# Kernel optimization log

Hardware: AMD Instinct MI355X
Metric: run time of the kernel (lower is better)

## Reference

```python
import jax, jax.numpy as jnp
import numpy as np

N_NODES = 100000
N_EDGES = 1600000
DK = 32
OUT_DIM = 32


def setup_inputs() -> dict:
    key = jax.random.key(0)
    ks = jax.random.split(key, 7)
    X = jax.random.normal(ks[0], (N_NODES, DK), dtype=jnp.float32)
    K = jax.random.normal(ks[1], (N_NODES, DK), dtype=jnp.float32)
    V = jax.random.normal(ks[2], (N_NODES, DK), dtype=jnp.float32)
    # output projection (nn.Dense(out_dim)) params
    W_o = jax.random.normal(ks[3], (DK, OUT_DIM), dtype=jnp.float32) / np.sqrt(DK)
    b_o = jnp.zeros((OUT_DIM,), dtype=jnp.float32)
    # sparsity descriptor td: edge list, dst sorted so segment ops see sorted ids
    src = jax.random.randint(ks[4], (N_EDGES,), 0, N_NODES, dtype=jnp.int32)
    dst = jnp.sort(jax.random.randint(ks[5], (N_EDGES,), 0, N_NODES, dtype=jnp.int32))
    return {"X": X, "K": K, "V": V, "W_o": W_o, "b_o": b_o,
            "src": src, "dst": dst, "num_seg": N_NODES}


def reference(X, K, V, W_o, b_o, src, dst, num_seg):
    dk = X.shape[-1]
    # per-edge attention logits: <Q[dst], K[src]> / dk  -> (E,)
    scores = jnp.einsum('ed,ed->e', jnp.take(X, dst, axis=0),
                        jnp.take(K, src, axis=0)) / dk
    # segment (per-neighborhood) softmax over edges sharing a dst node
    seg_max = jax.ops.segment_max(scores, dst, num_segments=num_seg,
                                  indices_are_sorted=True)
    e = jnp.exp(scores - jnp.take(seg_max, dst))
    denom = jax.ops.segment_sum(e, dst, num_segments=num_seg,
                                indices_are_sorted=True)
    alpha = e / jnp.take(denom, dst)  # (E,)
    # weighted aggregation of values, scattered back to nodes -> (N, dk)
    agg = jax.ops.segment_sum(alpha[:, None] * jnp.take(V, src, axis=0), dst,
                              num_segments=num_seg, indices_are_sorted=True)
    # output projection W_o
    return agg @ W_o + b_o
```

## Files before the change

kernel.cpp:

```cpp
#include <hip/hip_runtime.h>
#include <math.h>

#define DK 32
#define OUT_DIM 32

typedef float  f32x4  __attribute__((ext_vector_type(4)));
typedef short  bf16x8 __attribute__((ext_vector_type(8)));

__device__ __forceinline__ unsigned f2bf_rne(float x) {
    unsigned u = __float_as_uint(x);
    return (u + 0x7fffu + ((u >> 16) & 1u)) >> 16;
}

__global__ void prep_kernel(const int* __restrict__ dst,
                            const float* __restrict__ K,
                            const float* __restrict__ V,
                            int E, int N,
                            int* __restrict__ row_ptr,
                            unsigned* __restrict__ KV) {
    const int t = blockIdx.x * blockDim.x + threadIdx.x;
    if (t < E) {
        const int cur  = dst[t];
        const int prev = (t == 0) ? -1 : dst[t - 1];
        for (int j = prev + 1; j <= cur; ++j) row_ptr[j] = t;
        if (t == E - 1) {
            for (int j = cur + 1; j <= N; ++j) row_ptr[j] = E;
        }
    }
    if (t < N * DK) {
        KV[t] = (f2bf_rne(V[t]) << 16) | f2bf_rne(K[t]);
    }
}

__global__ void build_row_ptr_kernel(const int* __restrict__ dst, int E, int N,
                                     int* __restrict__ row_ptr) {
    int e = blockIdx.x * blockDim.x + threadIdx.x;
    if (e >= E) return;
    int cur  = dst[e];
    int prev = (e == 0) ? -1 : dst[e - 1];
    for (int j = prev + 1; j <= cur; ++j) row_ptr[j] = e;
    if (e == E - 1) {
        for (int j = cur + 1; j <= N; ++j) row_ptr[j] = E;
    }
}

__global__ __launch_bounds__(256) void gat_fused_kernel(
    const float* __restrict__ X, const uint4* __restrict__ KV,
    const float* __restrict__ Wo, const float* __restrict__ bo,
    const int* __restrict__ src, const int* __restrict__ row_ptr,
    float* __restrict__ out, int N) {

    __shared__ uint4 s_part[16 * 17];

    const int tid  = threadIdx.x;
    const int w    = tid >> 6;
    const int lane = tid & 63;
    const int g    = lane >> 3;
    const int c    = lane & 7;

    const int n_blk = blockIdx.x * 16;
    const int n_w   = n_blk + w * 4;

    const int rpv = row_ptr[min(n_w + min(lane, 4), N)];

    const float4* X4 = (const float4*)X;
    unsigned* part32 = (unsigned*)s_part;
    const float scale = 0.03125f;

    for (int i = 0; i < 4; ++i) {
        const int begin = __builtin_amdgcn_readlane(rpv, i);
        const int end   = __builtin_amdgcn_readlane(rpv, i + 1);
        const int n     = n_w + i;

        float4 q = X4[min(n, N - 1) * 8 + c];
        q.x *= scale; q.y *= scale; q.z *= scale; q.w *= scale;

        float  l   = 0.0f;
        float4 acc = make_float4(0.f, 0.f, 0.f, 0.f);

        for (int e0 = begin; e0 < end; e0 += 16) {
            const int sa = src[min(e0 + g,     end - 1)];
            const int sb = src[min(e0 + 8 + g, end - 1)];
            const uint4 A = KV[sa * 8 + c];
            const uint4 B = KV[sb * 8 + c];

            float p0 = fmaf(__uint_as_float(A.x << 16), q.x,
                       fmaf(__uint_as_float(A.y << 16), q.y,
                       fmaf(__uint_as_float(A.z << 16), q.z,
                            __uint_as_float(A.w << 16) * q.w)));
            float p1 = fmaf(__uint_as_float(B.x << 16), q.x,
                       fmaf(__uint_as_float(B.y << 16), q.y,
                       fmaf(__uint_as_float(B.z << 16), q.z,
                            __uint_as_float(B.w << 16) * q.w)));
            p0 += __shfl_xor(p0, 1);  p1 += __shfl_xor(p1, 1);
            p0 += __shfl_xor(p0, 2);  p1 += __shfl_xor(p1, 2);
            p0 += __shfl_xor(p0, 4);  p1 += __shfl_xor(p1, 4);

            const float w0 = (e0 + g     < end) ? __expf(p0) : 0.0f;
            const float w1 = (e0 + 8 + g < end) ? __expf(p1) : 0.0f;
            l += w0 + w1;

            acc.x = fmaf(w0, __uint_as_float(A.x & 0xffff0000u), acc.x);
            acc.y = fmaf(w0, __uint_as_float(A.y & 0xffff0000u), acc.y);
            acc.z = fmaf(w0, __uint_as_float(A.z & 0xffff0000u), acc.z);
            acc.w = fmaf(w0, __uint_as_float(A.w & 0xffff0000u), acc.w);
            acc.x = fmaf(w1, __uint_as_float(B.x & 0xffff0000u), acc.x);
            acc.y = fmaf(w1, __uint_as_float(B.y & 0xffff0000u), acc.y);
            acc.z = fmaf(w1, __uint_as_float(B.z & 0xffff0000u), acc.z);
            acc.w = fmaf(w1, __uint_as_float(B.w & 0xffff0000u), acc.w);
        }

        l     += __shfl_xor(l, 8);
        acc.x += __shfl_xor(acc.x, 8);  acc.y += __shfl_xor(acc.y, 8);
        acc.z += __shfl_xor(acc.z, 8);  acc.w += __shfl_xor(acc.w, 8);
        l += __shfl_xor(l, 16);  l += __shfl_xor(l, 32);

        const float inv = (end > begin) ? (1.0f / l) : 0.0f;
        acc.x *= inv; acc.y *= inv; acc.z *= inv; acc.w *= inv;

        if ((g & 1) == 0) {
            const int p   = g >> 1;
            const int row = w * 4 + i;
            const int off = row * 68 + p * 16 + c * 2;
            part32[off]     = f2bf_rne(acc.x) | (f2bf_rne(acc.y) << 16);
            part32[off + 1] = f2bf_rne(acc.z) | (f2bf_rne(acc.w) << 16);
        }
    }

    __syncthreads();

    if (w == 0) {
        const int quad = lane >> 4;
        const int col  = lane & 15;

        union BF { bf16x8 v; unsigned short u[8]; };
        BF bf0, bf1;
#pragma unroll
        for (int j2 = 0; j2 < 8; ++j2) {
            bf0.u[j2] = (unsigned short)f2bf_rne(Wo[(quad * 8 + j2) * OUT_DIM + col]);
            bf1.u[j2] = (unsigned short)f2bf_rne(Wo[(quad * 8 + j2) * OUT_DIM + 16 + col]);
        }
        const float bias0 = bo[col];
        const float bias1 = bo[16 + col];

        union AF { uint4 u; bf16x8 v; };
        f32x4 C0 = {bias0, bias0, bias0, bias0};
        f32x4 C1 = {bias1, bias1, bias1, bias1};
#pragma unroll
        for (int cc = 0; cc < 4; ++cc) {
            AF a;
            a.u = s_part[col * 17 + cc * 4 + quad];
            C0 = __builtin_amdgcn_mfma_f32_16x16x32_bf16(a.v, bf0.v, C0, 0, 0, 0);
            C1 = __builtin_amdgcn_mfma_f32_16x16x32_bf16(a.v, bf1.v, C1, 0, 0, 0);
        }
#pragma unroll
        for (int r = 0; r < 4; ++r) {
            const int n = n_blk + quad * 4 + r;
            if (n < N) {
                out[n * OUT_DIM + col]      = C0[r];
                out[n * OUT_DIM + 16 + col] = C1[r];
            }
        }
    }
}

__global__ __launch_bounds__(256) void gat_node_f32_kernel(
    const float* __restrict__ X, const float* __restrict__ Km,
    const float* __restrict__ Vm, const float* __restrict__ Wo,
    const float* __restrict__ bo, const int* __restrict__ src,
    const int* __restrict__ row_ptr, float* __restrict__ out, int N) {
    const int tid  = threadIdx.x;
    const int wave = tid >> 6;
    const int lane = tid & 63;
    const int g    = lane >> 3;
    const int c    = lane & 7;
    const int j    = lane & 31;
    const int half = lane >> 5;
    const int n = blockIdx.x * 4 + wave;
    if (n >= N) return;
    const int begin = row_ptr[n];
    const int end   = row_ptr[n + 1];
    const float4* X4 = (const float4*)X;
    const float4* K4 = (const float4*)Km;
    const float4* V4 = (const float4*)Vm;
    const float4 q4 = X4[n * 8 + c];
    float  l   = 0.0f;
    float4 acc = make_float4(0.0f, 0.0f, 0.0f, 0.0f);
    for (int e0 = begin; e0 < end; e0 += 16) {
        const int  ea = e0 + g;
        const int  eb = ea + 8;
        const bool va = ea < end;
        const bool vb = eb < end;
        const int sa = src[min(ea, end - 1)];
        const int sb = src[min(eb, end - 1)];
        const float4 ka  = K4[sa * 8 + c];
        const float4 kb  = K4[sb * 8 + c];
        const float4 vva = V4[sa * 8 + c];
        const float4 vvb = V4[sb * 8 + c];
        float pa = fmaf(ka.x, q4.x, fmaf(ka.y, q4.y, fmaf(ka.z, q4.z, ka.w * q4.w)));
        float pb = fmaf(kb.x, q4.x, fmaf(kb.y, q4.y, fmaf(kb.z, q4.z, kb.w * q4.w)));
        pa += __shfl_xor(pa, 1);  pb += __shfl_xor(pb, 1);
        pa += __shfl_xor(pa, 2);  pb += __shfl_xor(pb, 2);
        pa += __shfl_xor(pa, 4);  pb += __shfl_xor(pb, 4);
        const float wa = va ? __expf(pa * 0.03125f) : 0.0f;
        const float wb = vb ? __expf(pb * 0.03125f) : 0.0f;
        l += wa + wb;
        acc.x = fmaf(wa, vva.x, acc.x);  acc.y = fmaf(wa, vva.y, acc.y);
        acc.z = fmaf(wa, vva.z, acc.z);  acc.w = fmaf(wa, vva.w, acc.w);
        acc.x = fmaf(wb, vvb.x, acc.x);  acc.y = fmaf(wb, vvb.y, acc.y);
        acc.z = fmaf(wb, vvb.z, acc.z);  acc.w = fmaf(wb, vvb.w, acc.w);
    }
#pragma unroll
    for (int m = 8; m <= 32; m <<= 1) {
        l     += __shfl_xor(l, m);
        acc.x += __shfl_xor(acc.x, m);
        acc.y += __shfl_xor(acc.y, m);
        acc.z += __shfl_xor(acc.z, m);
        acc.w += __shfl_xor(acc.w, m);
    }
    const float inv = (end > begin) ? (1.0f / l) : 0.0f;
    float ag[4] = {acc.x, acc.y, acc.z, acc.w};
    float s = 0.0f;
#pragma unroll
    for (int k = 0; k < 32; ++k) {
        const float a = __int_as_float(
            __builtin_amdgcn_readlane(__float_as_int(ag[k & 3]), k >> 2));
        s = fmaf(a, Wo[k * OUT_DIM + j], s);
    }
    if (half == 0) {
        out[n * OUT_DIM + j] = fmaf(s, inv, bo[j]);
    }
}

extern "C" void kernel_launch(void* const* d_in, const int* in_sizes, int n_in,
                              void* d_out, int out_size, void* d_ws, size_t ws_size,
                              hipStream_t stream) {
    const float* X  = (const float*)d_in[0];
    const float* Km = (const float*)d_in[1];
    const float* Vm = (const float*)d_in[2];
    const float* Wo = (const float*)d_in[3];
    const float* bo = (const float*)d_in[4];
    const int* src  = (const int*)d_in[5];
    const int* dst  = (const int*)d_in[6];

    const int N = in_sizes[0] / DK;
    const int E = in_sizes[5];

    int* row_ptr = (int*)d_ws;
    const size_t kv_off = (((size_t)(N + 1) * 4) + 127) & ~(size_t)127;
    unsigned* KV = (unsigned*)((char*)d_ws + kv_off);
    const size_t need = kv_off + (size_t)N * DK * 4;
    float* out = (float*)d_out;

    const int tb = 256;

    if (ws_size >= need) {
        const int total  = N * DK;
        const int prep_n = (E > total) ? E : total;
        prep_kernel<<<(prep_n + tb - 1) / tb, tb, 0, stream>>>(dst, Km, Vm, E, N,
                                                               row_ptr, KV);
        const int grid = (N + 15) / 16;
        gat_fused_kernel<<<grid, 256, 0, stream>>>(X, (const uint4*)KV, Wo, bo,
                                                   src, row_ptr, out, N);
    } else {
        build_row_ptr_kernel<<<(E + tb - 1) / tb, tb, 0, stream>>>(dst, E, N, row_ptr);
        const int grid = (N + 3) / 4;
        gat_node_f32_kernel<<<grid, 256, 0, stream>>>(X, Km, Vm, Wo, bo,
                                                      src, row_ptr, out, N);
    }
}
```

Measured before the change: 140.8 us.

## Switch K/V packing and edge arithmetic from bf16 to fp16 with packed dot and FMA

```diff
diff --git a/kernel.cpp b/kernel.cpp
--- a/kernel.cpp
+++ b/kernel.cpp
@@ -4,12 +4,26 @@
 #define DK 32
 #define OUT_DIM 32
 
-typedef float  f32x4  __attribute__((ext_vector_type(4)));
-typedef short  bf16x8 __attribute__((ext_vector_type(8)));
-
-__device__ __forceinline__ unsigned f2bf_rne(float x) {
-    unsigned u = __float_as_uint(x);
-    return (u + 0x7fffu + ((u >> 16) & 1u)) >> 16;
+typedef float    f32x4 __attribute__((ext_vector_type(4)));
+typedef _Float16 h2    __attribute__((ext_vector_type(2)));
+typedef _Float16 h8    __attribute__((ext_vector_type(8)));
+
+#if __has_builtin(__builtin_amdgcn_fdot2)
+#define FDOT2(a, b, c) __builtin_amdgcn_fdot2((a), (b), (c), false)
+#else
+#define FDOT2(a, b, c) ((c) + (float)(a).x * (float)(b).x + (float)(a).y * (float)(b).y)
+#endif
+
+__device__ __forceinline__ h2 as_h2(unsigned u) {
+    union { unsigned u; h2 h; } v; v.u = u; return v.h;
+}
+__device__ __forceinline__ unsigned as_u32(h2 h) {
+    union { unsigned u; h2 h; } v; v.h = h; return v.u;
+}
+__device__ __forceinline__ h2 shfl_xor_h2(h2 v, int m) {
+    union { unsigned u; h2 h; } x; x.h = v;
+    x.u = (unsigned)__shfl_xor((int)x.u, m);
+    return x.h;
 }
 
 __global__ void prep_kernel(const int* __restrict__ dst,
@@ -17,7 +31,7 @@
                             const float* __restrict__ V,
                             int E, int N,
                             int* __restrict__ row_ptr,
-                            unsigned* __restrict__ KV) {
+                            unsigned* __restrict__ KVH) {
     const int t = blockIdx.x * blockDim.x + threadIdx.x;
     if (t < E) {
         const int cur  = dst[t];
@@ -28,7 +42,16 @@
         }
     }
     if (t < N * DK) {
-        KV[t] = (f2bf_rne(V[t]) << 16) | f2bf_rne(K[t]);
+        const int s = t >> 5;
+        const int r = t & 31;
+        const int c = r >> 2;
+        const int q = r & 3;
+        const float* srcp = (q < 2) ? K : V;
+        const int d0 = c * 4 + (q & 1) * 2;
+        h2 h;
+        h.x = (_Float16)srcp[s * DK + d0];
+        h.y = (_Float16)srcp[s * DK + d0 + 1];
+        KVH[t] = as_u32(h);
     }
 }
 
@@ -73,10 +96,12 @@
         const int n     = n_w + i;
 
         float4 q = X4[min(n, N - 1) * 8 + c];
-        q.x *= scale; q.y *= scale; q.z *= scale; q.w *= scale;
-
-        float  l   = 0.0f;
-        float4 acc = make_float4(0.f, 0.f, 0.f, 0.f);
+        h2 qh01, qh23;
+        qh01.x = (_Float16)(q.x * scale);  qh01.y = (_Float16)(q.y * scale);
+        qh23.x = (_Float16)(q.z * scale);  qh23.y = (_Float16)(q.w * scale);
+
+        float l = 0.0f;
+        h2 acc01 = (h2)0, acc23 = (h2)0;
 
         for (int e0 = begin; e0 < end; e0 += 16) {
             const int sa = src[min(e0 + g,     end - 1)];
@@ -84,14 +109,8 @@
             const uint4 A = KV[sa * 8 + c];
             const uint4 B = KV[sb * 8 + c];
 
-            float p0 = fmaf(__uint_as_float(A.x << 16), q.x,
-                       fmaf(__uint_as_float(A.y << 16), q.y,
-                       fmaf(__uint_as_float(A.z << 16), q.z,
-                            __uint_as_float(A.w << 16) * q.w)));
-            float p1 = fmaf(__uint_as_float(B.x << 16), q.x,
-                       fmaf(__uint_as_float(B.y << 16), q.y,
-                       fmaf(__uint_as_float(B.z << 16), q.z,
-                            __uint_as_float(B.w << 16) * q.w)));
+            float p0 = FDOT2(as_h2(A.y), qh23, FDOT2(as_h2(A.x), qh01, 0.0f));
+            float p1 = FDOT2(as_h2(B.y), qh23, FDOT2(as_h2(B.x), qh01, 0.0f));
             p0 += __shfl_xor(p0, 1);  p1 += __shfl_xor(p1, 1);
             p0 += __shfl_xor(p0, 2);  p1 += __shfl_xor(p1, 2);
             p0 += __shfl_xor(p0, 4);  p1 += __shfl_xor(p1, 4);
@@ -100,30 +119,30 @@
             const float w1 = (e0 + 8 + g < end) ? __expf(p1) : 0.0f;
             l += w0 + w1;
 
-            acc.x = fmaf(w0, __uint_as_float(A.x & 0xffff0000u), acc.x);
-            acc.y = fmaf(w0, __uint_as_float(A.y & 0xffff0000u), acc.y);
-            acc.z = fmaf(w0, __uint_as_float(A.z & 0xffff0000u), acc.z);
-            acc.w = fmaf(w0, __uint_as_float(A.w & 0xffff0000u), acc.w);
-            acc.x = fmaf(w1, __uint_as_float(B.x & 0xffff0000u), acc.x);
-            acc.y = fmaf(w1, __uint_as_float(B.y & 0xffff0000u), acc.y);
-            acc.z = fmaf(w1, __uint_as_float(B.z & 0xffff0000u), acc.z);
-            acc.w = fmaf(w1, __uint_as_float(B.w & 0xffff0000u), acc.w);
+            h2 wh0; wh0.x = (_Float16)w0; wh0.y = wh0.x;
+            h2 wh1; wh1.x = (_Float16)w1; wh1.y = wh1.x;
+            acc01 += wh0 * as_h2(A.z);
+            acc23 += wh0 * as_h2(A.w);
+            acc01 += wh1 * as_h2(B.z);
+            acc23 += wh1 * as_h2(B.w);
         }
 
         l     += __shfl_xor(l, 8);
-        acc.x += __shfl_xor(acc.x, 8);  acc.y += __shfl_xor(acc.y, 8);
-        acc.z += __shfl_xor(acc.z, 8);  acc.w += __shfl_xor(acc.w, 8);
+        acc01 += shfl_xor_h2(acc01, 8);
+        acc23 += shfl_xor_h2(acc23, 8);
         l += __shfl_xor(l, 16);  l += __shfl_xor(l, 32);
 
         const float inv = (end > begin) ? (1.0f / l) : 0.0f;
-        acc.x *= inv; acc.y *= inv; acc.z *= inv; acc.w *= inv;
+        h2 invh; invh.x = (_Float16)inv; invh.y = invh.x;
+        acc01 *= invh;
+        acc23 *= invh;
 
         if ((g & 1) == 0) {
             const int p   = g >> 1;
             const int row = w * 4 + i;
             const int off = row * 68 + p * 16 + c * 2;
-            part32[off]     = f2bf_rne(acc.x) | (f2bf_rne(acc.y) << 16);
-            part32[off + 1] = f2bf_rne(acc.z) | (f2bf_rne(acc.w) << 16);
+            part32[off]     = as_u32(acc01);
+            part32[off + 1] = as_u32(acc23);
         }
     }
 
@@ -133,25 +152,25 @@
         const int quad = lane >> 4;
         const int col  = lane & 15;
 
-        union BF { bf16x8 v; unsigned short u[8]; };
+        union BF { h8 v; _Float16 u[8]; };
         BF bf0, bf1;
 #pragma unroll
         for (int j2 = 0; j2 < 8; ++j2) {
-            bf0.u[j2] = (unsigned short)f2bf_rne(Wo[(quad * 8 + j2) * OUT_DIM + col]);
-            bf1.u[j2] = (unsigned short)f2bf_rne(Wo[(quad * 8 + j2) * OUT_DIM + 16 + col]);
+            bf0.u[j2] = (_Float16)Wo[(quad * 8 + j2) * OUT_DIM + col];
+            bf1.u[j2] = (_Float16)Wo[(quad * 8 + j2) * OUT_DIM + 16 + col];
         }
         const float bias0 = bo[col];
         const float bias1 = bo[16 + col];
 
-        union AF { uint4 u; bf16x8 v; };
+        union AF { uint4 u; h8 v; };
         f32x4 C0 = {bias0, bias0, bias0, bias0};
         f32x4 C1 = {bias1, bias1, bias1, bias1};
 #pragma unroll
         for (int cc = 0; cc < 4; ++cc) {
             AF a;
             a.u = s_part[col * 17 + cc * 4 + quad];
-            C0 = __builtin_amdgcn_mfma_f32_16x16x32_bf16(a.v, bf0.v, C0, 0, 0, 0);
-            C1 = __builtin_amdgcn_mfma_f32_16x16x32_bf16(a.v, bf1.v, C1, 0, 0, 0);
+            C0 = __builtin_amdgcn_mfma_f32_16x16x32_f16(a.v, bf0.v, C0, 0, 0, 0);
+            C1 = __builtin_amdgcn_mfma_f32_16x16x32_f16(a.v, bf1.v, C1, 0, 0, 0);
         }
 #pragma unroll
         for (int r = 0; r < 4; ++r) {
```

Result: no change. 143.2 us (+1.7%).
